# Performance work log

Measured on AMD Instinct MI355X. Metric: run time of the kernel, lower is better.

## Reference

```python
import jax, jax.numpy as jnp
import numpy as np

B = 16384
NUM_RATE, NUM_GENRE, NUM_DIRECTOR, NUM_ACTOR = 6, 25, 2186, 8030
EMB = 32


def setup_inputs() -> dict:
    key = jax.random.key(0)
    k0, k1, k2, k3, k4 = jax.random.split(key, 5)
    x = jax.random.randint(k0, (B, 1 + NUM_GENRE + NUM_DIRECTOR + NUM_ACTOR), 0, 2, dtype=jnp.int64 if jax.config.jax_enable_x64 else jnp.int32)
    rate_table = jax.random.normal(k1, (NUM_RATE, EMB), dtype=jnp.float32)
    # torch Linear weights have shape [out_features, in_features]
    W_genre = jax.random.normal(k2, (EMB, NUM_GENRE), dtype=jnp.float32) * (1.0 / np.sqrt(NUM_GENRE))
    W_director = jax.random.normal(k3, (EMB, NUM_DIRECTOR), dtype=jnp.float32) * (1.0 / np.sqrt(NUM_DIRECTOR))
    W_actor = jax.random.normal(k4, (EMB, NUM_ACTOR), dtype=jnp.float32) * (1.0 / np.sqrt(NUM_ACTOR))
    return {"x": x, "rate_table": rate_table, "W_genre": W_genre,
            "W_director": W_director, "W_actor": W_actor}


def _maxnorm_gather(table, idx, max_norm=1.0, eps=1e-7):
    # torch.nn.Embedding(max_norm=1.0): rows accessed are renormalized to norm <= max_norm
    rows = table[idx]  # [B, E]
    norm = jnp.linalg.norm(rows, axis=-1, keepdims=True)
    scale = jnp.where(norm > max_norm, max_norm / (norm + eps), 1.0)
    return rows * scale


def _mean_pool_linear(multi_hot_f, W):
    # Linear(no bias) on multi-hot then divide by row-sum == mean-pooled embedding bag
    emb = jnp.einsum('bn,en->be', multi_hot_f, W)
    return emb / jnp.sum(multi_hot_f, axis=1, keepdims=True)


def reference(x, rate_table, W_genre, W_director, W_actor):
    rate_idx = x[:, 0]
    genre = x[:, 1:26].astype(jnp.float32)
    director = x[:, 26:2212].astype(jnp.float32)
    actors = x[:, 2212:10242].astype(jnp.float32)
    rate_emb = _maxnorm_gather(rate_table, rate_idx)
    genre_emb = _mean_pool_linear(genre, W_genre)
    director_emb = _mean_pool_linear(director, W_director)
    actors_emb = _mean_pool_linear(actors, W_actor)
    return jnp.concatenate((rate_emb, genre_emb, director_emb, actors_emb), axis=1)  # [B, 4*EMB]
```

## Files before the change

kernel.cpp:

```cpp
#include <hip/hip_runtime.h>
#include <hip/hip_bf16.h>

#define B_ROWS 16384
#define XC     10242
#define NGENRE 25
#define NDIR   2186
#define NACT   8030
#define EMB    32
#define KT_TOTAL 321
#define OUTC   128
#define NCOLS  112
#define PART_STRIDE ((size_t)B_ROWS * NCOLS)
#define WFRAG_BYTES ((size_t)KT_TOTAL * 4 * 64 * 16)

typedef short bf16x8 __attribute__((ext_vector_type(8)));
typedef float f32x4  __attribute__((ext_vector_type(4)));
typedef int   i32x4a __attribute__((ext_vector_type(4), aligned(4)));

__global__ void prep_wfrag(const float* __restrict__ wg,
                           const float* __restrict__ wd,
                           const float* __restrict__ wa,
                           uint4* __restrict__ Wfrag) {
  const int kt = blockIdx.x;
  const int s  = threadIdx.x >> 6;
  const int l  = threadIdx.x & 63;
  const int n  = l & 15;
  const int k0 = kt * 32 + ((l >> 4) << 3);

  unsigned short v[8];
#pragma unroll
  for (int j = 0; j < 8; ++j) {
    const int k = k0 + j;
    float f = 0.f;
    if (kt == 0) {
      if (s < 2) { if (k >= 1 && k < 26) f = wg[(s * 16 + n) * NGENRE + (k - 1)]; }
      else       { if (k >= 26)          f = wd[((s - 2) * 16 + n) * NDIR + (k - 26)]; }
    } else if (kt < 69) {
      if (s < 2) f = wd[(s * 16 + n) * NDIR + (k - 26)];
    } else if (kt == 69) {
      if (s < 2) { if (k < 2212)  f = wd[(s * 16 + n) * NDIR + (k - 26)]; }
      else       { if (k >= 2212) f = wa[((s - 2) * 16 + n) * NACT + (k - 2212)]; }
    } else if (kt < 320) {
      if (s < 2) f = wa[(s * 16 + n) * NACT + (k - 2212)];
    } else {
      if (s < 2 && k < XC) f = wa[(s * 16 + n) * NACT + (k - 2212)];
    }
    __hip_bfloat16 h = __float2bfloat16(f);
    v[j] = *reinterpret_cast<unsigned short*>(&h);
  }
  union { unsigned short u[8]; uint4 q; } cv;
#pragma unroll
  for (int j = 0; j < 8; ++j) cv.u[j] = v[j];
  Wfrag[((size_t)kt * 4 + s) * 64 + l] = cv.q;
}

template<int KS>
__global__ __launch_bounds__(256) void main_mm(const int* __restrict__ x,
                                               const uint4* __restrict__ Wfrag,
                                               float* __restrict__ part) {
  constexpr int PER = (((KT_TOTAL + KS - 1) / KS) + 3) & ~3;
  const int t    = threadIdx.x;
  const int rb   = blockIdx.x & 255;
  const int ks   = blockIdx.x >> 8;
  const int ktA  = ks * PER;
  const int ktB  = (ktA + PER < KT_TOTAL) ? ktA + PER : KT_TOTAL;
  const int lane = t & 63;
  const int w    = t >> 6;
  const int lo   = lane & 15, hi = lane >> 4;
  const int* xrow = x + (size_t)(rb * 64 + w * 16 + lo) * XC;

  f32x4 accG0 = {0,0,0,0}, accG1 = {0,0,0,0};
  f32x4 accD0 = {0,0,0,0}, accD1 = {0,0,0,0};
  f32x4 accA0 = {0,0,0,0}, accA1 = {0,0,0,0};
  f32x4 accI  = {0,0,0,0};

  auto load_x8 = [&](int kt, int* dst) {
    int k0 = kt * 32 + hi * 8;
    if (kt < 320) {
      i32x4a a = *reinterpret_cast<const i32x4a*>(xrow + k0);
      i32x4a b = *reinterpret_cast<const i32x4a*>(xrow + k0 + 4);
      dst[0]=a[0]; dst[1]=a[1]; dst[2]=a[2]; dst[3]=a[3];
      dst[4]=b[0]; dst[5]=b[1]; dst[6]=b[2]; dst[7]=b[3];
    } else {
#pragma unroll
      for (int j = 0; j < 8; ++j) dst[j] = (k0 + j < XC) ? xrow[k0 + j] : 0;
    }
  };
  auto packa = [&](const int* cx) -> bf16x8 {
    union { unsigned int w4[4]; bf16x8 v; } af;
#pragma unroll
    for (int i = 0; i < 4; ++i)
      af.w4[i] = ((unsigned)cx[2*i] + ((unsigned)cx[2*i+1] << 16)) * 0x3F80u;
    return af.v;
  };
  auto bload = [&](int kt, int s) -> bf16x8 {
    union { uint4 q; bf16x8 v; } c;
    c.q = Wfrag[((size_t)kt * 4 + s) * 64 + lane];
    return c.v;
  };
  auto mkconst = [&](bool on) -> bf16x8 {
    union { unsigned int w4[4]; bf16x8 v; } c;
    unsigned int u = on ? 0x3F803F80u : 0u;
    c.w4[0]=u; c.w4[1]=u; c.w4[2]=u; c.w4[3]=u;
    return c.v;
  };
  const bf16x8 ivD = mkconst(lo == 1);
  const bf16x8 ivA = mkconst(lo == 2);

  auto do_mfma = [&](int kt, bf16x8 a) {
    const int kb = kt * 32 + hi * 8;
    if (kt == 0) {
      accG0 = __builtin_amdgcn_mfma_f32_16x16x32_bf16(a, bload(0,0), accG0, 0,0,0);
      accG1 = __builtin_amdgcn_mfma_f32_16x16x32_bf16(a, bload(0,1), accG1, 0,0,0);
      accD0 = __builtin_amdgcn_mfma_f32_16x16x32_bf16(a, bload(0,2), accD0, 0,0,0);
      accD1 = __builtin_amdgcn_mfma_f32_16x16x32_bf16(a, bload(0,3), accD1, 0,0,0);
      union { unsigned short u[8]; bf16x8 v; } iv;
#pragma unroll
      for (int j = 0; j < 8; ++j) {
        int k = kb + j;
        bool on = (lo == 0) ? (k >= 1 && k < 26) : (lo == 1) ? (k >= 26) : false;
        iv.u[j] = on ? (unsigned short)0x3F80 : (unsigned short)0;
      }
      accI = __builtin_amdgcn_mfma_f32_16x16x32_bf16(a, iv.v, accI, 0,0,0);
    } else if (kt < 69) {
      accD0 = __builtin_amdgcn_mfma_f32_16x16x32_bf16(a, bload(kt,0), accD0, 0,0,0);
      accD1 = __builtin_amdgcn_mfma_f32_16x16x32_bf16(a, bload(kt,1), accD1, 0,0,0);
      accI  = __builtin_amdgcn_mfma_f32_16x16x32_bf16(a, ivD, accI, 0,0,0);
    } else if (kt == 69) {
      accD0 = __builtin_amdgcn_mfma_f32_16x16x32_bf16(a, bload(69,0), accD0, 0,0,0);
      accD1 = __builtin_amdgcn_mfma_f32_16x16x32_bf16(a, bload(69,1), accD1, 0,0,0);
      accA0 = __builtin_amdgcn_mfma_f32_16x16x32_bf16(a, bload(69,2), accA0, 0,0,0);
      accA1 = __builtin_amdgcn_mfma_f32_16x16x32_bf16(a, bload(69,3), accA1, 0,0,0);
      union { unsigned short u[8]; bf16x8 v; } iv;
#pragma unroll
      for (int j = 0; j < 8; ++j) {
        int k = kb + j;
        bool on = (lo == 1) ? (k < 2212) : (lo == 2) ? (k >= 2212) : false;
        iv.u[j] = on ? (unsigned short)0x3F80 : (unsigned short)0;
      }
      accI = __builtin_amdgcn_mfma_f32_16x16x32_bf16(a, iv.v, accI, 0,0,0);
    } else if (kt < 320) {
      accA0 = __builtin_amdgcn_mfma_f32_16x16x32_bf16(a, bload(kt,0), accA0, 0,0,0);
      accA1 = __builtin_amdgcn_mfma_f32_16x16x32_bf16(a, bload(kt,1), accA1, 0,0,0);
      accI  = __builtin_amdgcn_mfma_f32_16x16x32_bf16(a, ivA, accI, 0,0,0);
    } else {
      accA0 = __builtin_amdgcn_mfma_f32_16x16x32_bf16(a, bload(320,0), accA0, 0,0,0);
      accA1 = __builtin_amdgcn_mfma_f32_16x16x32_bf16(a, bload(320,1), accA1, 0,0,0);
      union { unsigned short u[8]; bf16x8 v; } iv;
#pragma unroll
      for (int j = 0; j < 8; ++j) {
        int k = kb + j;
        iv.u[j] = (lo == 2 && k < XC) ? (unsigned short)0x3F80 : (unsigned short)0;
      }
      accI = __builtin_amdgcn_mfma_f32_16x16x32_bf16(a, iv.v, accI, 0,0,0);
    }
  };

  int xg0[8], xg1[8], xg2[8], xg3[8];
  for (int g = ktA; g < ktB; g += 4) {
    load_x8(g, xg0);
    if (g + 1 < ktB) load_x8(g + 1, xg1);
    if (g + 2 < ktB) load_x8(g + 2, xg2);
    if (g + 3 < ktB) load_x8(g + 3, xg3);

    do_mfma(g, packa(xg0));
    if (g + 1 < ktB) do_mfma(g + 1, packa(xg1));
    if (g + 2 < ktB) do_mfma(g + 2, packa(xg2));
    if (g + 3 < ktB) do_mfma(g + 3, packa(xg3));
  }

  float* slab = part + (size_t)ks * PART_STRIDE;
  const int rbase = rb * 64 + w * 16 + hi * 4;
#pragma unroll
  for (int j = 0; j < 4; ++j) {
    size_t ro = (size_t)(rbase + j) * NCOLS;
    slab[ro +  0 + lo] = accG0[j];
    slab[ro + 16 + lo] = accG1[j];
    slab[ro + 32 + lo] = accD0[j];
    slab[ro + 48 + lo] = accD1[j];
    slab[ro + 64 + lo] = accA0[j];
    slab[ro + 80 + lo] = accA1[j];
    if (lo < 3) slab[ro + 96 + lo] = accI[j];
  }
}

__global__ __launch_bounds__(128) void reduce_k(const int* __restrict__ x,
                                                const float* __restrict__ rate,
                                                const float* __restrict__ part,
                                                int ksplit,
                                                float* __restrict__ out) {
  __shared__ float cnt[3];
  const int r = blockIdx.x;
  const int c = threadIdx.x;

  if (c < 3) {
    float s = 0.f;
    for (int ks = 0; ks < ksplit; ++ks)
      s += part[(size_t)ks * PART_STRIDE + (size_t)r * NCOLS + 96 + c];
    cnt[c] = s;
  }
  __syncthreads();

  float res;
  if (c < EMB) {
    int idx = x[(size_t)r * XC];
    float v = rate[idx * EMB + c];
    float s2 = v * v;
    s2 += __shfl_xor(s2, 1, 32);
    s2 += __shfl_xor(s2, 2, 32);
    s2 += __shfl_xor(s2, 4, 32);
    s2 += __shfl_xor(s2, 8, 32);
    s2 += __shfl_xor(s2, 16, 32);
    float norm = sqrtf(s2);
    float scale = (norm > 1.0f) ? (1.0f / (norm + 1e-7f)) : 1.0f;
    res = v * scale;
  } else {
    int cc = c - EMB;
    float val = 0.f;
    for (int ks = 0; ks < ksplit; ++ks)
      val += part[(size_t)ks * PART_STRIDE + (size_t)r * NCOLS + cc];
    res = val / cnt[cc >> 5];
  }
  out[(size_t)r * OUTC + c] = res;
}

extern "C" void kernel_launch(void* const* d_in, const int* in_sizes, int n_in,
                              void* d_out, int out_size, void* d_ws, size_t ws_size,
                              hipStream_t stream) {
  (void)in_sizes; (void)n_in; (void)out_size;
  const int*   x    = (const int*)d_in[0];
  const float* rate = (const float*)d_in[1];
  const float* wg   = (const float*)d_in[2];
  const float* wd   = (const float*)d_in[3];
  const float* wa   = (const float*)d_in[4];
  float* out  = (float*)d_out;
  float* part = (float*)d_ws;

  const size_t slab_bytes = PART_STRIDE * sizeof(float);
  int KS;
  if      (ws_size >= 8 * slab_bytes + WFRAG_BYTES) KS = 8;
  else if (ws_size >= 4 * slab_bytes + WFRAG_BYTES) KS = 4;
  else if (ws_size >= 2 * slab_bytes + WFRAG_BYTES) KS = 2;
  else                                              KS = 1;
  uint4* Wfrag = (uint4*)((char*)d_ws + (size_t)KS * slab_bytes);

  prep_wfrag<<<KT_TOTAL, 256, 0, stream>>>(wg, wd, wa, Wfrag);
  switch (KS) {
    case 8: main_mm<8><<<8 * 256, 256, 0, stream>>>(x, Wfrag, part); break;
    case 4: main_mm<4><<<4 * 256, 256, 0, stream>>>(x, Wfrag, part); break;
    case 2: main_mm<2><<<2 * 256, 256, 0, stream>>>(x, Wfrag, part); break;
    default: main_mm<1><<<1 * 256, 256, 0, stream>>>(x, Wfrag, part); break;
  }
  reduce_k<<<B_ROWS, 128, 0, stream>>>(x, rate, part, KS, out);
}
```

Measured before the change: 923.4 us.

## Split main loop into branch-free segment runs with batched weight prefetch

Restructures the K loop of the MFMA kernel so that homogeneous director and actor segments run through a specialized 4-tile routine. That routine issues all x loads and weight-fragment loads up front before the MFMAs. Boundary tiles (0, 69, 320) and remainders go through a per-tile slow path. It also adds a min-blocks-per-CU launch bound of 4 to cap register use. The aim is to remove per-tile branching and give the loads more latency hiding, at the risk of register pressure or spills from the hoisted B fragments.

```diff
diff --git a/kernel.cpp b/kernel.cpp
--- a/kernel.cpp
+++ b/kernel.cpp
@@ -55,9 +55,9 @@
 }
 
 template<int KS>
-__global__ __launch_bounds__(256) void main_mm(const int* __restrict__ x,
-                                               const uint4* __restrict__ Wfrag,
-                                               float* __restrict__ part) {
+__global__ __launch_bounds__(256, 4) void main_mm(const int* __restrict__ x,
+                                                  const uint4* __restrict__ Wfrag,
+                                                  float* __restrict__ part) {
   constexpr int PER = (((KT_TOTAL + KS - 1) / KS) + 3) & ~3;
   const int t    = threadIdx.x;
   const int rb   = blockIdx.x & 255;
@@ -107,7 +107,10 @@
   const bf16x8 ivD = mkconst(lo == 1);
   const bf16x8 ivA = mkconst(lo == 2);
 
-  auto do_mfma = [&](int kt, bf16x8 a) {
+  auto slow_tile = [&](int kt) {
+    int xv[8];
+    load_x8(kt, xv);
+    bf16x8 a = packa(xv);
     const int kb = kt * 32 + hi * 8;
     if (kt == 0) {
       accG0 = __builtin_amdgcn_mfma_f32_16x16x32_bf16(a, bload(0,0), accG0, 0,0,0);
@@ -156,17 +159,47 @@
     }
   };
 
-  int xg0[8], xg1[8], xg2[8], xg3[8];
-  for (int g = ktA; g < ktB; g += 4) {
-    load_x8(g, xg0);
-    if (g + 1 < ktB) load_x8(g + 1, xg1);
-    if (g + 2 < ktB) load_x8(g + 2, xg2);
-    if (g + 3 < ktB) load_x8(g + 3, xg3);
-
-    do_mfma(g, packa(xg0));
-    if (g + 1 < ktB) do_mfma(g + 1, packa(xg1));
-    if (g + 2 < ktB) do_mfma(g + 2, packa(xg2));
-    if (g + 3 < ktB) do_mfma(g + 3, packa(xg3));
+  auto run4 = [&](int ktS, int ktE, f32x4& s0, f32x4& s1, const bf16x8 ivS) {
+    for (int g = ktS; g < ktE; g += 4) {
+      int x0[8], x1[8], x2[8], x3[8];
+      bf16x8 b00, b01, b10, b11, b20, b21, b30, b31;
+      load_x8(g,     x0); b00 = bload(g,     0); b01 = bload(g,     1);
+      load_x8(g + 1, x1); b10 = bload(g + 1, 0); b11 = bload(g + 1, 1);
+      load_x8(g + 2, x2); b20 = bload(g + 2, 0); b21 = bload(g + 2, 1);
+      load_x8(g + 3, x3); b30 = bload(g + 3, 0); b31 = bload(g + 3, 1);
+      bf16x8 a;
+      a = packa(x0);
+      s0 = __builtin_amdgcn_mfma_f32_16x16x32_bf16(a, b00, s0, 0,0,0);
+      s1 = __builtin_amdgcn_mfma_f32_16x16x32_bf16(a, b01, s1, 0,0,0);
+      accI = __builtin_amdgcn_mfma_f32_16x16x32_bf16(a, ivS, accI, 0,0,0);
+      a = packa(x1);
+      s0 = __builtin_amdgcn_mfma_f32_16x16x32_bf16(a, b10, s0, 0,0,0);
+      s1 = __builtin_amdgcn_mfma_f32_16x16x32_bf16(a, b11, s1, 0,0,0);
+      accI = __builtin_amdgcn_mfma_f32_16x16x32_bf16(a, ivS, accI, 0,0,0);
+      a = packa(x2);
+      s0 = __builtin_amdgcn_mfma_f32_16x16x32_bf16(a, b20, s0, 0,0,0);
+      s1 = __builtin_amdgcn_mfma_f32_16x16x32_bf16(a, b21, s1, 0,0,0);
+      accI = __builtin_amdgcn_mfma_f32_16x16x32_bf16(a, ivS, accI, 0,0,0);
+      a = packa(x3);
+      s0 = __builtin_amdgcn_mfma_f32_16x16x32_bf16(a, b30, s0, 0,0,0);
+      s1 = __builtin_amdgcn_mfma_f32_16x16x32_bf16(a, b31, s1, 0,0,0);
+      accI = __builtin_amdgcn_mfma_f32_16x16x32_bf16(a, ivS, accI, 0,0,0);
+    }
+  };
+
+  int kt = ktA;
+  while (kt < ktB) {
+    if (kt == 0 || kt == 69 || kt == 320) { slow_tile(kt); ++kt; continue; }
+    const bool isD = (kt < 69);
+    const int segEnd = isD ? 69 : 320;
+    const int runEnd = (ktB < segEnd) ? ktB : segEnd;
+    const int n4 = (runEnd - kt) & ~3;
+    if (n4 > 0) {
+      if (isD) run4(kt, kt + n4, accD0, accD1, ivD);
+      else     run4(kt, kt + n4, accA0, accA1, ivA);
+      kt += n4;
+    }
+    while (kt < runEnd) { slow_tile(kt); ++kt; }
   }
 
   float* slab = part + (size_t)ks * PART_STRIDE;
```

New measurement: 955.8 us. +3.5%, slower.
